# Kernel tuning notes

Hardware: AMD Instinct MI355X
Metric: run time of the kernel (lower is better)

Reference implementation:

```python
import jax, jax.numpy as jnp
import numpy as np

T, B, S = 64, 128, 128
H = 200   # hidden_size
E = 200   # embedding_size
A = 100   # attention projection width
V = 10003 # vocab_size


def setup_inputs() -> dict:
    key = jax.random.key(0)
    ks = jax.random.split(key, 20)
    def n(k, shape, scale):
        return (jax.random.normal(k, shape, jnp.float32) * scale).astype(jnp.float32)
    return {
        "tokens": jax.random.randint(ks[0], (T, B), 0, V),
        "hidden": n(ks[1], (1, B, H), 0.1),
        "encoder_outputs": n(ks[2], (S, B, H), 1.0),
        "emb": n(ks[3], (V, E), 0.05),
        "W1": n(ks[4], (A, H), 0.07), "b1": n(ks[5], (A,), 0.07),
        "W2": n(ks[6], (A, H), 0.07), "b2": n(ks[7], (A,), 0.07),
        "W3": n(ks[8], (A, E), 0.07), "b3": n(ks[9], (A,), 0.07),
        "attn_W": n(ks[10], (1, A), 0.1), "attn_b": n(ks[11], (1,), 0.1),
        "gru_Wih": n(ks[12], (3 * H, E + H), 0.05), "gru_Whh": n(ks[13], (3 * H, H), 0.05),
        "gru_bih": n(ks[14], (3 * H,), 0.05), "gru_bhh": n(ks[15], (3 * H,), 0.05),
        "out_W": n(ks[16], (V, H), 0.05), "out_b": n(ks[17], (V,), 0.05),
    }


def reference(tokens, hidden, encoder_outputs, emb, W1, b1, W2, b2, W3, b3,
              attn_W, attn_b, gru_Wih, gru_Whh, gru_bih, gru_bhh, out_W, out_b):
    # eval mode: dropout is identity
    enc = jnp.transpose(encoder_outputs, (1, 0, 2))   # [B, S, H]
    embedded = emb[tokens]                            # [T, B, E]
    ah3 = embedded @ W3.T + b3                        # [T, B, A] (precomputed, as in torch)
    ah2 = enc @ W2.T + b2                             # [B, S, A]
    h0 = hidden[0]                                    # [B, H]

    def step(h, xs):
        emb_t, ah3_t = xs                             # [B,E], [B,A]
        ah1 = h @ W1.T + b1                           # [B, A]
        e = jax.nn.relu(ah1[:, None, :] + ah2 + ah3_t[:, None, :])  # [B, S, A]
        logits = (e @ attn_W.T + attn_b)[..., 0]      # [B, S]
        a = jax.nn.softmax(logits, axis=1)            # [B, S]
        ctx = jnp.einsum('bs,bsh->bh', a, enc)        # [B, H]
        x = jnp.concatenate([emb_t, ctx], axis=1)     # [B, E+H]
        gi = x @ gru_Wih.T + gru_bih                  # [B, 3H]
        gh = h @ gru_Whh.T + gru_bhh                  # [B, 3H]
        ir, iz, in_ = jnp.split(gi, 3, axis=1)
        hr, hz, hn = jnp.split(gh, 3, axis=1)
        r = jax.nn.sigmoid(ir + hr)
        z = jax.nn.sigmoid(iz + hz)
        nn_ = jnp.tanh(in_ + r * hn)
        h_new = (1.0 - z) * nn_ + z * h               # [B, H]
        logp = jax.nn.log_softmax(h_new @ out_W.T + out_b, axis=1)  # [B, V]
        return h_new, (logp, a)

    h_last, (outputs, attns) = jax.lax.scan(step, h0, (embedded, ah3))
    # outputs [T,B,V]; hidden [1,B,H]; attentions [T,B,1,S] (torch's view(B,1,S) per step)
    return outputs, h_last[None], attns[:, :, None, :]
```

## Files before the change

### kernel.cpp

```cpp
#include <hip/hip_runtime.h>
#include <hip/hip_bf16.h>
#include <cmath>

constexpr int T_ = 64, B_ = 128, S_ = 128, H_ = 200, E_ = 200, A_ = 100, V_ = 10003;
constexpr int KP = 224;
constexpr int VP = 10240;
constexpr int MROWS = T_ * B_;
constexpr int NCB = VP / 256;
constexpr int G3 = 3 * H_;
constexpr int EH = E_ + H_;
constexpr int ELD = 136;
constexpr int AH2P = 104;
constexpr int NP = 768;

typedef __attribute__((ext_vector_type(8))) short bf16x8;
typedef __attribute__((ext_vector_type(4))) float f32x4;
typedef __attribute__((ext_vector_type(2))) _Float16 h2;
typedef __attribute__((ext_vector_type(8))) _Float16 h8;

#if __has_builtin(__builtin_amdgcn_fdot2)
__device__ __forceinline__ float fdot2f(h2 a, h2 b, float c) {
  return __builtin_amdgcn_fdot2(a, b, c, false);
}
#else
__device__ __forceinline__ float fdot2f(h2 a, h2 b, float c) {
  return c + (float)a[0] * (float)b[0] + (float)a[1] * (float)b[1];
}
#endif

__device__ __forceinline__ float dot200p5(const h8* __restrict__ w, int stride,
                                          const h8* __restrict__ x) {
  const h8* p = w;
  h8 w0 = p[0]; p += stride;
  h8 w1 = p[0]; p += stride;
  h8 w2 = p[0]; p += stride;
  h8 w3 = p[0]; p += stride;
  h8 w4 = p[0]; p += stride;
  float a0 = 0.f, a1 = 0.f, a2 = 0.f, a3 = 0.f;
#define DOT_CONSUME(WREG, K)                    \
  {                                             \
    h8 xv = x[K];                               \
    h2 wp[4], xp[4];                            \
    __builtin_memcpy(wp, &WREG, 16);            \
    __builtin_memcpy(xp, &xv, 16);              \
    a0 = fdot2f(wp[0], xp[0], a0);              \
    a1 = fdot2f(wp[1], xp[1], a1);              \
    a2 = fdot2f(wp[2], xp[2], a2);              \
    a3 = fdot2f(wp[3], xp[3], a3);              \
  }
#define DOT_RELOAD(WREG) { WREG = p[0]; p += stride; }
  DOT_CONSUME(w0, 0)  DOT_RELOAD(w0)
  DOT_CONSUME(w1, 1)  DOT_RELOAD(w1)
  DOT_CONSUME(w2, 2)  DOT_RELOAD(w2)
  DOT_CONSUME(w3, 3)  DOT_RELOAD(w3)
  DOT_CONSUME(w4, 4)  DOT_RELOAD(w4)
  DOT_CONSUME(w0, 5)  DOT_RELOAD(w0)
  DOT_CONSUME(w1, 6)  DOT_RELOAD(w1)
  DOT_CONSUME(w2, 7)  DOT_RELOAD(w2)
  DOT_CONSUME(w3, 8)  DOT_RELOAD(w3)
  DOT_CONSUME(w4, 9)  DOT_RELOAD(w4)
  DOT_CONSUME(w0, 10) DOT_RELOAD(w0)
  DOT_CONSUME(w1, 11) DOT_RELOAD(w1)
  DOT_CONSUME(w2, 12) DOT_RELOAD(w2)
  DOT_CONSUME(w3, 13) DOT_RELOAD(w3)
  DOT_CONSUME(w4, 14) DOT_RELOAD(w4)
  DOT_CONSUME(w0, 15) DOT_RELOAD(w0)
  DOT_CONSUME(w1, 16) DOT_RELOAD(w1)
  DOT_CONSUME(w2, 17) DOT_RELOAD(w2)
  DOT_CONSUME(w3, 18) DOT_RELOAD(w3)
  DOT_CONSUME(w4, 19) DOT_RELOAD(w4)
  DOT_CONSUME(w0, 20)
  DOT_CONSUME(w1, 21)
  DOT_CONSUME(w2, 22)
  DOT_CONSUME(w3, 23)
  DOT_CONSUME(w4, 24)
#undef DOT_CONSUME
#undef DOT_RELOAD
  return (a0 + a1) + (a2 + a3);
}


__global__ __launch_bounds__(256) void k_pack(const float* __restrict__ outW,
                                              const float* __restrict__ W1,
                                              const float* __restrict__ Wih,
                                              const float* __restrict__ Whh,
                                              const float* __restrict__ W3,
                                              __hip_bfloat16* __restrict__ wpk,
                                              __hip_bfloat16* __restrict__ hall,
                                              _Float16* __restrict__ W1h,
                                              _Float16* __restrict__ Wihh,
                                              _Float16* __restrict__ Whhh,
                                              __hip_bfloat16* __restrict__ wep) {
  const int stride = gridDim.x * blockDim.x;
  const int tid0 = blockIdx.x * blockDim.x + threadIdx.x;
  const int total = (KP / 8) * VP * 8;
  for (int idx = tid0; idx < total; idx += stride) {
    int kk = idx & 7;
    int v = (idx >> 3) % VP;
    int kb = idx / (8 * VP);
    int k = kb * 8 + kk;
    float val = (k < H_ && v < V_) ? outW[(size_t)v * H_ + k] : 0.f;
    wpk[idx] = __float2bfloat16(val);
  }
  const __hip_bfloat16 z = __float2bfloat16(0.f);
  for (int idx = tid0; idx < MROWS * (KP - H_); idx += stride) {
    int row = idx / (KP - H_), col = H_ + idx % (KP - H_);
    hall[(size_t)row * KP + col] = z;
  }
  for (int idx = tid0; idx < 25 * A_ * 8; idx += stride) {
    int kk = idx & 7, a = (idx >> 3) % A_, k8 = idx / (8 * A_);
    W1h[idx] = (_Float16)W1[(size_t)a * H_ + k8 * 8 + kk];
  }
  for (int idx = tid0; idx < 50 * G3 * 8; idx += stride) {
    int kk = idx & 7, n = (idx >> 3) % G3, k8 = idx / (8 * G3);
    Wihh[idx] = (_Float16)Wih[(size_t)n * EH + k8 * 8 + kk];
  }
  for (int idx = tid0; idx < 25 * G3 * 8; idx += stride) {
    int kk = idx & 7, n = (idx >> 3) % G3, k8 = idx / (8 * G3);
    Whhh[idx] = (_Float16)Whh[(size_t)n * H_ + k8 * 8 + kk];
  }
  for (int idx = tid0; idx < (KP / 8) * NP * 8; idx += stride) {
    int kk = idx & 7, c = (idx >> 3) % NP, k8 = idx / (8 * NP);
    int k = k8 * 8 + kk;
    float v = 0.f;
    if (k < E_) {
      if (c < G3) v = Wih[(size_t)c * EH + k];
      else if (c < G3 + A_) v = W3[(size_t)(c - G3) * E_ + k];
    }
    wep[idx] = __float2bfloat16(v);
  }
}

__global__ __launch_bounds__(256) void k_ah2(const float* __restrict__ encoder,
                                             const float* __restrict__ W2,
                                             const float* __restrict__ b2,
                                             _Float16* __restrict__ ah2h) {
  __shared__ float encL[16][200];
  const int s = blockIdx.x, b0 = blockIdx.y * 16, tid = threadIdx.x;
  for (int i = tid; i < 16 * 200; i += 256) {
    int bl = i / 200, k = i % 200;
    encL[bl][k] = encoder[((size_t)s * B_ + b0 + bl) * H_ + k];
  }
  __syncthreads();
  for (int o = tid; o < 16 * A_; o += 256) {
    int bl = o / A_, a = o % A_;
    const float* w = W2 + (size_t)a * H_;
    float acc = b2[a];
    for (int k = 0; k < H_; ++k) acc += encL[bl][k] * w[k];
    ah2h[((size_t)(b0 + bl) * S_ + s) * AH2P + a] = (_Float16)acc;
  }
  for (int o = tid; o < 16 * (AH2P - A_); o += 256) {
    int bl = o / (AH2P - A_), a = A_ + o % (AH2P - A_);
    ah2h[((size_t)(b0 + bl) * S_ + s) * AH2P + a] = (_Float16)0.f;
  }
}

__global__ __launch_bounds__(256) void k_gemb(const int* __restrict__ tokens,
                                              const float* __restrict__ emb,
                                              const short* __restrict__ wep,
                                              const float* __restrict__ bih,
                                              const float* __restrict__ b3,
                                              float* __restrict__ giX,
                                              float* __restrict__ ah3) {
  constexpr int ALD = 232;
  __shared__ __align__(16) __hip_bfloat16 aL[64 * ALD];
  __shared__ int tokL[64];
  const int tid = threadIdx.x;
  const int w = tid >> 6, l = tid & 63, lm = l & 15, lg = l >> 4;
  const int r0 = blockIdx.y * 64;
  const int v0 = blockIdx.x * 256 + w * 64;

  if (tid < 64) tokL[tid] = tokens[r0 + tid];
  __syncthreads();
  for (int i = tid; i < 64 * KP; i += 256) {
    int row = i / KP, k = i - row * KP;
    float v = (k < E_) ? emb[(size_t)tokL[row] * E_ + k] : 0.f;
    aL[row * ALD + k] = __float2bfloat16(v);
  }
  __syncthreads();

  f32x4 acc[4][4] = {};
#pragma unroll
  for (int kt = 0; kt < KP / 32; ++kt) {
    const int k0 = kt * 32;
    bf16x8 af[4], bfr[4];
#pragma unroll
    for (int wm = 0; wm < 4; ++wm)
      af[wm] = *(const bf16x8*)(aL + (wm * 16 + lm) * ALD + k0 + lg * 8);
#pragma unroll
    for (int n = 0; n < 4; ++n)
      bfr[n] = *(const bf16x8*)(wep + ((size_t)((k0 >> 3) + lg) * NP + v0 + n * 16 + lm) * 8);
#pragma unroll
    for (int wm = 0; wm < 4; ++wm)
#pragma unroll
      for (int n = 0; n < 4; ++n)
        acc[wm][n] = __builtin_amdgcn_mfma_f32_16x16x32_bf16(af[wm], bfr[n], acc[wm][n], 0, 0, 0);
  }

#pragma unroll
  for (int n = 0; n < 4; ++n) {
    const int vv = v0 + n * 16 + lm;
    const bool isGi = vv < G3;
    const bool isA3 = !isGi && vv < G3 + A_;
    const float bias = isGi ? bih[vv] : (isA3 ? b3[vv - G3] : 0.f);
#pragma unroll
    for (int wm = 0; wm < 4; ++wm) {
#pragma unroll
      for (int j = 0; j < 4; ++j) {
        const int row = r0 + wm * 16 + lg * 4 + j;
        const float val = acc[wm][n][j] + bias;
        if (isGi) giX[(size_t)row * G3 + vv] = val;
        else if (isA3) ah3[(size_t)row * A_ + (vv - G3)] = val;
      }
    }
  }
}

__global__ __launch_bounds__(512) void k_recur(const float* __restrict__ hidden0,
                                               const _Float16* __restrict__ ah2h,
                                               const float* __restrict__ ah3,
                                               const float* __restrict__ encoder,
                                               const _Float16* __restrict__ W1h,
                                               const float* __restrict__ b1,
                                               const float* __restrict__ attn_W,
                                               const float* __restrict__ attn_b,
                                               const _Float16* __restrict__ Wihh,
                                               const _Float16* __restrict__ Whhh,
                                               const float* __restrict__ bhh,
                                               const float* __restrict__ giX,
                                               __hip_bfloat16* __restrict__ hall,
                                               float* __restrict__ out_hidden,
                                               float* __restrict__ out_attn) {
  __shared__ __align__(16) _Float16 encLh[H_ * ELD];
  __shared__ __align__(16) h2 h16[100];
  __shared__ __align__(16) h2 xch[100];
  __shared__ __align__(16) h2 aLh[64];
  __shared__ float s1[AH2P];
  __shared__ float aW[AH2P];
  __shared__ float red[8];
  __shared__ float giL[G3];
  __shared__ float part[1200];

  const int b = blockIdx.x, tid = threadIdx.x;
  const int lane = tid & 63;

  for (int i = tid; i < S_ * H_; i += 512) {
    int s = i / H_, h = i - s * H_;
    encLh[h * ELD + s] = (_Float16)encoder[((size_t)s * B_ + b) * H_ + h];
  }
  float hreg = 0.f, bhr = 0.f, bhz = 0.f, bhn = 0.f;
  if (tid < H_) {
    hreg = hidden0[b * H_ + tid];
    bhr = bhh[tid]; bhz = bhh[200 + tid]; bhn = bhh[400 + tid];
  }
  if (tid < 100) {
    h2 v;
    v[0] = (_Float16)hidden0[b * H_ + 2 * tid];
    v[1] = (_Float16)hidden0[b * H_ + 2 * tid + 1];
    h16[tid] = v;
  }
  for (int i = tid; i < AH2P; i += 512) {
    aW[i] = (i < A_) ? attn_W[i] : 0.f;
    s1[i] = 0.f;
  }
  h8 ah2row[13];
  if (tid < S_) {
    const h8* src = (const h8*)(ah2h + ((size_t)b * S_ + tid) * AH2P);
#pragma unroll
    for (int r = 0; r < 13; ++r) ah2row[r] = src[r];
  }
  const float ab = attn_b[0];
  __syncthreads();

  const h8* W1h8 = (const h8*)W1h;
  const h8* Wihc8 = (const h8*)Wihh + (size_t)25 * G3;
  const h8* Whhh8 = (const h8*)Whhh;

  for (int t = 0; t < T_; ++t) {
    const h8* xs = (const h8*)h16;
    for (int u = tid; u < 700; u += 512) {
      if (u < 100) {
        const float ah3A = ah3[((size_t)t * B_ + b) * A_ + u];
        const float b1A = b1[u];
        s1[u] = dot200p5(W1h8 + u, A_, xs) + b1A + ah3A;
      } else {
        const int g = u - 100;
        part[g] = dot200p5(Whhh8 + g, G3, xs);
      }
    }
    __syncthreads();

    float evw = 0.f;
    const int w01 = tid >> 6;
    if (tid < S_) {
      float acc = ab;
#pragma unroll
      for (int r = 0; r < 13; ++r) {
        h8 w = ah2row[r];
#pragma unroll
        for (int j = 0; j < 8; ++j) {
          const int a = r * 8 + j;
          acc += fmaxf(s1[a] + (float)w[j], 0.f) * aW[a];
        }
      }
      float m = acc;
#pragma unroll
      for (int off = 32; off > 0; off >>= 1) m = fmaxf(m, __shfl_xor(m, off, 64));
      evw = expf(acc - m);
      float sm = evw;
#pragma unroll
      for (int off = 32; off > 0; off >>= 1) sm += __shfl_xor(sm, off, 64);
      if (lane == 0) { red[w01] = m; red[4 + w01] = sm; }
    }
    __syncthreads();
    if (tid < S_) {
      const float m0 = red[0], m1 = red[1];
      const float M = fmaxf(m0, m1);
      const float SS = red[4] * expf(m0 - M) + red[5] * expf(m1 - M);
      const float av = evw * expf((w01 ? m1 : m0) - M) / SS;
      out_attn[((size_t)t * B_ + b) * S_ + tid] = av;
      const float avn = __shfl_xor(av, 1, 64);
      if ((tid & 1) == 0) {
        h2 v; v[0] = (_Float16)av; v[1] = (_Float16)avn;
        aLh[tid >> 1] = v;
      }
    }
    __syncthreads();

    if (tid < H_) {
      const h8* er = (const h8*)(encLh + tid * ELD);
      float c0 = 0.f, c1 = 0.f, c2 = 0.f, c3 = 0.f;
#pragma unroll
      for (int k8 = 0; k8 < 16; ++k8) {
        h8 evv = er[k8];
        h2 ep[4];
        __builtin_memcpy(ep, &evv, 16);
        c0 = fdot2f(ep[0], aLh[4 * k8 + 0], c0);
        c1 = fdot2f(ep[1], aLh[4 * k8 + 1], c1);
        c2 = fdot2f(ep[2], aLh[4 * k8 + 2], c2);
        c3 = fdot2f(ep[3], aLh[4 * k8 + 3], c3);
      }
      const float c = (c0 + c1) + (c2 + c3);
      const float cn = __shfl_xor(c, 1, 64);
      if ((tid & 1) == 0) {
        h2 v; v[0] = (_Float16)c; v[1] = (_Float16)cn;
        xch[tid >> 1] = v;
      }
    } else {
      const int j = tid - 200;
      if (j < 300) {
        float2 g2 = ((const float2*)(giX + ((size_t)t * B_ + b) * G3))[j];
        giL[2 * j] = g2.x;
        giL[2 * j + 1] = g2.y;
      }
    }
    __syncthreads();

    {
      const h8* xc8 = (const h8*)xch;
      for (int u = tid; u < 600; u += 512) {
        part[600 + u] = dot200p5(Wihc8 + u, G3, xc8);
      }
    }
    __syncthreads();

    if (tid < H_) {
      const int n = tid;
      const float gir = giL[n] + part[600 + n];
      const float giz = giL[200 + n] + part[800 + n];
      const float gin = giL[400 + n] + part[1000 + n];
      const float ghr = part[n] + bhr;
      const float ghz = part[200 + n] + bhz;
      const float ghn = part[400 + n] + bhn;
      const float r = 1.f / (1.f + expf(-(gir + ghr)));
      const float z = 1.f / (1.f + expf(-(giz + ghz)));
      const float nn = tanhf(gin + r * ghn);
      const float hv = (1.f - z) * nn + z * hreg;
      hreg = hv;
      hall[((size_t)t * B_ + b) * KP + n] = __float2bfloat16(hv);
      const float hn2 = __shfl_xor(hv, 1, 64);
      if ((n & 1) == 0) {
        h2 v; v[0] = (_Float16)hv; v[1] = (_Float16)hn2;
        h16[n >> 1] = v;
      }
      if (t == T_ - 1) out_hidden[b * H_ + n] = hv;
    }
    __syncthreads();
  }
}

__global__ __launch_bounds__(256) void k_big0(const short* __restrict__ hb,
                                              const short* __restrict__ wpk,
                                              const float* __restrict__ outb,
                                              float* __restrict__ pmax,
                                              float* __restrict__ psum) {
  const int tid = threadIdx.x;
  const int w = tid >> 6, l = tid & 63;
  const int lm = l & 15, lg = l >> 4;
  const int r0 = blockIdx.y * 64;
  const int v0 = blockIdx.x * 256 + w * 64;

  f32x4 acc[4][4] = {};
#pragma unroll
  for (int kt = 0; kt < KP / 32; ++kt) {
    const int k0 = kt * 32;
    bf16x8 af[4], bfr[4];
#pragma unroll
    for (int wm = 0; wm < 4; ++wm)
      af[wm] = *(const bf16x8*)(hb + (size_t)(r0 + wm * 16 + lm) * KP + k0 + lg * 8);
#pragma unroll
    for (int n = 0; n < 4; ++n)
      bfr[n] = *(const bf16x8*)(wpk + ((size_t)((k0 >> 3) + lg) * VP + v0 + n * 16 + lm) * 8);
#pragma unroll
    for (int wm = 0; wm < 4; ++wm)
#pragma unroll
      for (int n = 0; n < 4; ++n)
        acc[wm][n] = __builtin_amdgcn_mfma_f32_16x16x32_bf16(af[wm], bfr[n], acc[wm][n], 0, 0, 0);
  }

  int vv[4]; float bias[4]; bool val[4];
#pragma unroll
  for (int n = 0; n < 4; ++n) {
    vv[n] = v0 + n * 16 + lm;
    val[n] = vv[n] < V_;
    bias[n] = val[n] ? outb[vv[n]] : 0.f;
  }

  __shared__ float smax[4][64], ssum[4][64];
#pragma unroll
  for (int wm = 0; wm < 4; ++wm) {
#pragma unroll
    for (int j = 0; j < 4; ++j) {
      float mv = -INFINITY;
#pragma unroll
      for (int n = 0; n < 4; ++n)
        if (val[n]) mv = fmaxf(mv, acc[wm][n][j] + bias[n]);
      for (int off = 8; off > 0; off >>= 1) mv = fmaxf(mv, __shfl_xor(mv, off, 64));
      float sv = 0.f;
#pragma unroll
      for (int n = 0; n < 4; ++n)
        if (val[n]) sv += expf(acc[wm][n][j] + bias[n] - mv);
      for (int off = 8; off > 0; off >>= 1) sv += __shfl_xor(sv, off, 64);
      if (lm == 0) {
        smax[w][wm * 16 + lg * 4 + j] = mv;
        ssum[w][wm * 16 + lg * 4 + j] = sv;
      }
    }
  }
  __syncthreads();
  if (tid < 64) {
    float mv = -INFINITY;
    for (int ww = 0; ww < 4; ++ww) mv = fmaxf(mv, smax[ww][tid]);
    float sv = 0.f;
    for (int ww = 0; ww < 4; ++ww) {
      float sw = ssum[ww][tid];
      if (sw > 0.f) sv += expf(smax[ww][tid] - mv) * sw;
    }
    pmax[(size_t)blockIdx.x * MROWS + r0 + tid] = mv;
    psum[(size_t)blockIdx.x * MROWS + r0 + tid] = sv;
  }
}

__global__ __launch_bounds__(256) void k_lse(const float* __restrict__ pmax,
                                             const float* __restrict__ psum,
                                             float* __restrict__ lse) {
  const int r = blockIdx.x * 256 + threadIdx.x;
  float mv = -INFINITY;
  for (int c = 0; c < NCB; ++c) mv = fmaxf(mv, pmax[(size_t)c * MROWS + r]);
  float sv = 0.f;
  for (int c = 0; c < NCB; ++c) {
    float sw = psum[(size_t)c * MROWS + r];
    if (sw > 0.f) sv += expf(pmax[(size_t)c * MROWS + r] - mv) * sw;
  }
  lse[r] = mv + logf(sv);
}

__global__ __launch_bounds__(256) void k_big1(const short* __restrict__ hb,
                                              const short* __restrict__ wpk,
                                              const float* __restrict__ outb,
                                              const float* __restrict__ lse,
                                              float* __restrict__ out_logp) {
  const int tid = threadIdx.x;
  const int w = tid >> 6, l = tid & 63;
  const int lm = l & 15, lg = l >> 4;
  const int r0 = blockIdx.y * 64;
  const int v0 = blockIdx.x * 256 + w * 64;

  __shared__ float lseL[64];
  if (tid < 64) lseL[tid] = lse[r0 + tid];

  f32x4 acc[4][4] = {};
#pragma unroll
  for (int kt = 0; kt < KP / 32; ++kt) {
    const int k0 = kt * 32;
    bf16x8 af[4], bfr[4];
#pragma unroll
    for (int wm = 0; wm < 4; ++wm)
      af[wm] = *(const bf16x8*)(hb + (size_t)(r0 + wm * 16 + lm) * KP + k0 + lg * 8);
#pragma unroll
    for (int n = 0; n < 4; ++n)
      bfr[n] = *(const bf16x8*)(wpk + ((size_t)((k0 >> 3) + lg) * VP + v0 + n * 16 + lm) * 8);
#pragma unroll
    for (int wm = 0; wm < 4; ++wm)
#pragma unroll
      for (int n = 0; n < 4; ++n)
        acc[wm][n] = __builtin_amdgcn_mfma_f32_16x16x32_bf16(af[wm], bfr[n], acc[wm][n], 0, 0, 0);
  }

  int vv[4]; float bias[4]; bool val[4];
#pragma unroll
  for (int n = 0; n < 4; ++n) {
    vv[n] = v0 + n * 16 + lm;
    val[n] = vv[n] < V_;
    bias[n] = val[n] ? outb[vv[n]] : 0.f;
  }
  __syncthreads();
#pragma unroll
  for (int wm = 0; wm < 4; ++wm) {
#pragma unroll
    for (int j = 0; j < 4; ++j) {
      const int row = r0 + wm * 16 + lg * 4 + j;
      const float ls = lseL[wm * 16 + lg * 4 + j];
#pragma unroll
      for (int n = 0; n < 4; ++n)
        if (val[n]) out_logp[(size_t)row * V_ + vv[n]] = acc[wm][n][j] + bias[n] - ls;
    }
  }
}


extern "C" void kernel_launch(void* const* d_in, const int* in_sizes, int n_in,
                              void* d_out, int out_size, void* d_ws, size_t ws_size,
                              hipStream_t stream) {
  (void)in_sizes; (void)n_in; (void)out_size; (void)ws_size;
  const int* tokens = (const int*)d_in[0];
  const float* hidden0 = (const float*)d_in[1];
  const float* encoder = (const float*)d_in[2];
  const float* emb = (const float*)d_in[3];
  const float* W1 = (const float*)d_in[4];
  const float* b1 = (const float*)d_in[5];
  const float* W2 = (const float*)d_in[6];
  const float* b2 = (const float*)d_in[7];
  const float* W3 = (const float*)d_in[8];
  const float* b3 = (const float*)d_in[9];
  const float* attn_W = (const float*)d_in[10];
  const float* attn_b = (const float*)d_in[11];
  const float* Wih = (const float*)d_in[12];
  const float* Whh = (const float*)d_in[13];
  const float* bih = (const float*)d_in[14];
  const float* bhh = (const float*)d_in[15];
  const float* outW = (const float*)d_in[16];
  const float* outb = (const float*)d_in[17];

  float* out_logp = (float*)d_out;
  float* out_hidden = out_logp + (size_t)T_ * B_ * V_;
  float* out_attn = out_hidden + (size_t)B_ * H_;

  float* ws = (float*)d_ws;
  float* ah3w = ws;
  float* pmaxw = ah3w + (size_t)T_ * B_ * A_;
  float* psumw = pmaxw + (size_t)NCB * MROWS;
  float* lsew = psumw + (size_t)NCB * MROWS;
  float* giXw = lsew + MROWS;
  __hip_bfloat16* hallw = (__hip_bfloat16*)(giXw + (size_t)MROWS * G3);
  __hip_bfloat16* wpkw = hallw + (size_t)MROWS * KP;
  _Float16* ah2hw = (_Float16*)(wpkw + (size_t)(KP / 8) * VP * 8);
  _Float16* W1hw = ah2hw + (size_t)B_ * S_ * AH2P;
  _Float16* Wihhw = W1hw + (size_t)25 * A_ * 8;
  _Float16* Whhhw = Wihhw + (size_t)50 * G3 * 8;
  __hip_bfloat16* wepw = (__hip_bfloat16*)(Whhhw + (size_t)25 * G3 * 8);

  k_pack<<<512, 256, 0, stream>>>(outW, W1, Wih, Whh, W3, wpkw, hallw,
                                  W1hw, Wihhw, Whhhw, wepw);
  k_ah2<<<dim3(S_, B_ / 16), 256, 0, stream>>>(encoder, W2, b2, ah2hw);
  k_gemb<<<dim3(NP / 256, MROWS / 64), 256, 0, stream>>>(tokens, emb, (const short*)wepw,
                                                         bih, b3, giXw, ah3w);

  k_recur<<<B_, 512, 0, stream>>>(hidden0, ah2hw, ah3w, encoder, W1hw, b1, attn_W,
                                  attn_b, Wihhw, Whhhw, bhh, giXw,
                                  hallw, out_hidden, out_attn);

  k_big0<<<dim3(NCB, MROWS / 64), 256, 0, stream>>>((const short*)hallw, (const short*)wpkw,
                                                    outb, pmaxw, psumw);
  k_lse<<<MROWS / 256, 256, 0, stream>>>(pmaxw, psumw, lsew);
  k_big1<<<dim3(NCB, MROWS / 64), 256, 0, stream>>>((const short*)hallw, (const short*)wpkw,
                                                    outb, lsew, out_logp);
}
```

Baseline: 1.033 ms.

## Overlap output-weight packing with recurrence and widen recurrent block to 640 threads

Moves the packing of the large output projection weights and the zeroing of hall padding out of k_pack and into 32 extra blocks of k_recur, so this work runs on otherwise idle CUs while the 128 serial recurrence blocks execute. The recurrence block grows from 512 to 640 threads, so each phase maps one unit per thread with no second strided pass. The leftover Whh gate dot products are computed by spare threads during the attention phase, and giX is loaded as float4. The risks are higher register pressure from the larger block and contention between the packing blocks and the recurrence for memory bandwidth.

```diff
diff --git a/kernel.cpp b/kernel.cpp
--- a/kernel.cpp
+++ b/kernel.cpp
@@ -12,6 +12,8 @@
 constexpr int ELD = 136;
 constexpr int AH2P = 104;
 constexpr int NP = 768;
+constexpr int NTH = 640;
+constexpr int NPK = 32;
 
 typedef __attribute__((ext_vector_type(8))) short bf16x8;
 typedef __attribute__((ext_vector_type(4))) float f32x4;
@@ -80,33 +82,16 @@
 }
 
 
-__global__ __launch_bounds__(256) void k_pack(const float* __restrict__ outW,
-                                              const float* __restrict__ W1,
+__global__ __launch_bounds__(256) void k_pack(const float* __restrict__ W1,
                                               const float* __restrict__ Wih,
                                               const float* __restrict__ Whh,
                                               const float* __restrict__ W3,
-                                              __hip_bfloat16* __restrict__ wpk,
-                                              __hip_bfloat16* __restrict__ hall,
                                               _Float16* __restrict__ W1h,
                                               _Float16* __restrict__ Wihh,
                                               _Float16* __restrict__ Whhh,
                                               __hip_bfloat16* __restrict__ wep) {
   const int stride = gridDim.x * blockDim.x;
   const int tid0 = blockIdx.x * blockDim.x + threadIdx.x;
-  const int total = (KP / 8) * VP * 8;
-  for (int idx = tid0; idx < total; idx += stride) {
-    int kk = idx & 7;
-    int v = (idx >> 3) % VP;
-    int kb = idx / (8 * VP);
-    int k = kb * 8 + kk;
-    float val = (k < H_ && v < V_) ? outW[(size_t)v * H_ + k] : 0.f;
-    wpk[idx] = __float2bfloat16(val);
-  }
-  const __hip_bfloat16 z = __float2bfloat16(0.f);
-  for (int idx = tid0; idx < MROWS * (KP - H_); idx += stride) {
-    int row = idx / (KP - H_), col = H_ + idx % (KP - H_);
-    hall[(size_t)row * KP + col] = z;
-  }
   for (int idx = tid0; idx < 25 * A_ * 8; idx += stride) {
     int kk = idx & 7, a = (idx >> 3) % A_, k8 = idx / (8 * A_);
     W1h[idx] = (_Float16)W1[(size_t)a * H_ + k8 * 8 + kk];
@@ -216,7 +201,7 @@
   }
 }
 
-__global__ __launch_bounds__(512) void k_recur(const float* __restrict__ hidden0,
+__global__ __launch_bounds__(NTH) void k_recur(const float* __restrict__ hidden0,
                                                const _Float16* __restrict__ ah2h,
                                                const float* __restrict__ ah3,
                                                const float* __restrict__ encoder,
@@ -228,6 +213,8 @@
                                                const _Float16* __restrict__ Whhh,
                                                const float* __restrict__ bhh,
                                                const float* __restrict__ giX,
+                                               const float* __restrict__ outW,
+                                               __hip_bfloat16* __restrict__ wpk,
                                                __hip_bfloat16* __restrict__ hall,
                                                float* __restrict__ out_hidden,
                                                float* __restrict__ out_attn) {
@@ -244,7 +231,27 @@
   const int b = blockIdx.x, tid = threadIdx.x;
   const int lane = tid & 63;
 
-  for (int i = tid; i < S_ * H_; i += 512) {
+  if (b >= B_) {
+    const int pt = (b - B_) * NTH + tid;
+    const int pstride = NPK * NTH;
+    const int total = (KP / 8) * VP * 8;
+    for (int idx = pt; idx < total; idx += pstride) {
+      int kk = idx & 7;
+      int v = (idx >> 3) % VP;
+      int kb = idx / (8 * VP);
+      int k = kb * 8 + kk;
+      float val = (k < H_ && v < V_) ? outW[(size_t)v * H_ + k] : 0.f;
+      wpk[idx] = __float2bfloat16(val);
+    }
+    const __hip_bfloat16 z = __float2bfloat16(0.f);
+    for (int idx = pt; idx < MROWS * (KP - H_); idx += pstride) {
+      int row = idx / (KP - H_), col = H_ + idx % (KP - H_);
+      hall[(size_t)row * KP + col] = z;
+    }
+    return;
+  }
+
+  for (int i = tid; i < S_ * H_; i += NTH) {
     int s = i / H_, h = i - s * H_;
     encLh[h * ELD + s] = (_Float16)encoder[((size_t)s * B_ + b) * H_ + h];
   }
@@ -259,7 +266,7 @@
     v[1] = (_Float16)hidden0[b * H_ + 2 * tid + 1];
     h16[tid] = v;
   }
-  for (int i = tid; i < AH2P; i += 512) {
+  for (int i = tid; i < AH2P; i += NTH) {
     aW[i] = (i < A_) ? attn_W[i] : 0.f;
     s1[i] = 0.f;
   }
@@ -278,15 +285,13 @@
 
   for (int t = 0; t < T_; ++t) {
     const h8* xs = (const h8*)h16;
-    for (int u = tid; u < 700; u += 512) {
-      if (u < 100) {
-        const float ah3A = ah3[((size_t)t * B_ + b) * A_ + u];
-        const float b1A = b1[u];
-        s1[u] = dot200p5(W1h8 + u, A_, xs) + b1A + ah3A;
-      } else {
-        const int g = u - 100;
-        part[g] = dot200p5(Whhh8 + g, G3, xs);
-      }
+    if (tid < 100) {
+      const float ah3A = ah3[((size_t)t * B_ + b) * A_ + tid];
+      const float b1A = b1[tid];
+      s1[tid] = dot200p5(W1h8 + tid, A_, xs) + b1A + ah3A;
+    } else {
+      const int g = tid - 100;
+      part[g] = dot200p5(Whhh8 + g, G3, xs);
     }
     __syncthreads();
 
@@ -346,21 +351,21 @@
         h2 v; v[0] = (_Float16)c; v[1] = (_Float16)cn;
         xch[tid >> 1] = v;
       }
-    } else {
+    } else if (tid < 350) {
       const int j = tid - 200;
-      if (j < 300) {
-        float2 g2 = ((const float2*)(giX + ((size_t)t * B_ + b) * G3))[j];
-        giL[2 * j] = g2.x;
-        giL[2 * j + 1] = g2.y;
-      }
+      float4 g4 = ((const float4*)(giX + ((size_t)t * B_ + b) * G3))[j];
+      giL[4 * j] = g4.x;
+      giL[4 * j + 1] = g4.y;
+      giL[4 * j + 2] = g4.z;
+      giL[4 * j + 3] = g4.w;
+    } else if (tid < 410) {
+      const int g = 540 + (tid - 350);
+      part[g] = dot200p5(Whhh8 + g, G3, xs);
     }
     __syncthreads();
 
-    {
-      const h8* xc8 = (const h8*)xch;
-      for (int u = tid; u < 600; u += 512) {
-        part[600 + u] = dot200p5(Wihc8 + u, G3, xc8);
-      }
+    if (tid < 600) {
+      part[600 + tid] = dot200p5(Wihc8 + tid, G3, (const h8*)xch);
     }
     __syncthreads();
 
@@ -570,15 +575,14 @@
   _Float16* Whhhw = Wihhw + (size_t)50 * G3 * 8;
   __hip_bfloat16* wepw = (__hip_bfloat16*)(Whhhw + (size_t)25 * G3 * 8);
 
-  k_pack<<<512, 256, 0, stream>>>(outW, W1, Wih, Whh, W3, wpkw, hallw,
-                                  W1hw, Wihhw, Whhhw, wepw);
+  k_pack<<<256, 256, 0, stream>>>(W1, Wih, Whh, W3, W1hw, Wihhw, Whhhw, wepw);
   k_ah2<<<dim3(S_, B_ / 16), 256, 0, stream>>>(encoder, W2, b2, ah2hw);
   k_gemb<<<dim3(NP / 256, MROWS / 64), 256, 0, stream>>>(tokens, emb, (const short*)wepw,
                                                          bih, b3, giXw, ah3w);
 
-  k_recur<<<B_, 512, 0, stream>>>(hidden0, ah2hw, ah3w, encoder, W1hw, b1, attn_W,
-                                  attn_b, Wihhw, Whhhw, bhh, giXw,
-                                  hallw, out_hidden, out_attn);
+  k_recur<<<B_ + NPK, NTH, 0, stream>>>(hidden0, ah2hw, ah3w, encoder, W1hw, b1, attn_W,
+                                        attn_b, Wihhw, Whhhw, bhh, giXw, outW, wpkw,
+                                        hallw, out_hidden, out_attn);
 
   k_big0<<<dim3(NCB, MROWS / 64), 256, 0, stream>>>((const short*)hallw, (const short*)wpkw,
                                                     outb, pmaxw, psumw);
```

Result: slower. 2.109 ms (+104.1%).

## Overlap output-weight packing with recurrence and use MFMA for encoder projection

Applied to the files above, without the earlier changes.

Packing of the large output-projection weights and zero-padding of the hidden buffer move out of the pre-pass kernel into 32 extra blocks of the recurrence kernel, so that work runs alongside the latency-bound recurrent loop. The scalar-FMA encoder projection kernel (ah2) is replaced with a bf16 MFMA GEMM over packed W2. This trades some precision (bf16 instead of fp32 for ah2) and adds packing blocks that compete with the recurrence blocks for resources.

```diff
diff --git a/kernel.cpp b/kernel.cpp
--- a/kernel.cpp
+++ b/kernel.cpp
@@ -12,6 +12,9 @@
 constexpr int ELD = 136;
 constexpr int AH2P = 104;
 constexpr int NP = 768;
+constexpr int NP2 = 128;
+constexpr int NTH = 512;
+constexpr int NPK = 32;
 
 typedef __attribute__((ext_vector_type(8))) short bf16x8;
 typedef __attribute__((ext_vector_type(4))) float f32x4;
@@ -80,33 +83,19 @@
 }
 
 
-__global__ __launch_bounds__(256) void k_pack(const float* __restrict__ outW,
-                                              const float* __restrict__ W1,
+__global__ __launch_bounds__(256) void k_pack(const float* __restrict__ W1,
                                               const float* __restrict__ Wih,
                                               const float* __restrict__ Whh,
                                               const float* __restrict__ W3,
-                                              __hip_bfloat16* __restrict__ wpk,
-                                              __hip_bfloat16* __restrict__ hall,
+                                              const float* __restrict__ W2,
                                               _Float16* __restrict__ W1h,
                                               _Float16* __restrict__ Wihh,
                                               _Float16* __restrict__ Whhh,
-                                              __hip_bfloat16* __restrict__ wep) {
+                                              __hip_bfloat16* __restrict__ wep,
+                                              __hip_bfloat16* __restrict__ w2p,
+                                              _Float16* __restrict__ ah2h) {
   const int stride = gridDim.x * blockDim.x;
   const int tid0 = blockIdx.x * blockDim.x + threadIdx.x;
-  const int total = (KP / 8) * VP * 8;
-  for (int idx = tid0; idx < total; idx += stride) {
-    int kk = idx & 7;
-    int v = (idx >> 3) % VP;
-    int kb = idx / (8 * VP);
-    int k = kb * 8 + kk;
-    float val = (k < H_ && v < V_) ? outW[(size_t)v * H_ + k] : 0.f;
-    wpk[idx] = __float2bfloat16(val);
-  }
-  const __hip_bfloat16 z = __float2bfloat16(0.f);
-  for (int idx = tid0; idx < MROWS * (KP - H_); idx += stride) {
-    int row = idx / (KP - H_), col = H_ + idx % (KP - H_);
-    hall[(size_t)row * KP + col] = z;
-  }
   for (int idx = tid0; idx < 25 * A_ * 8; idx += stride) {
     int kk = idx & 7, a = (idx >> 3) % A_, k8 = idx / (8 * A_);
     W1h[idx] = (_Float16)W1[(size_t)a * H_ + k8 * 8 + kk];
@@ -129,29 +118,70 @@
     }
     wep[idx] = __float2bfloat16(v);
   }
-}
-
-__global__ __launch_bounds__(256) void k_ah2(const float* __restrict__ encoder,
-                                             const float* __restrict__ W2,
-                                             const float* __restrict__ b2,
-                                             _Float16* __restrict__ ah2h) {
-  __shared__ float encL[16][200];
-  const int s = blockIdx.x, b0 = blockIdx.y * 16, tid = threadIdx.x;
-  for (int i = tid; i < 16 * 200; i += 256) {
-    int bl = i / 200, k = i % 200;
-    encL[bl][k] = encoder[((size_t)s * B_ + b0 + bl) * H_ + k];
+  for (int idx = tid0; idx < (KP / 8) * NP2 * 8; idx += stride) {
+    int kk = idx & 7, c = (idx >> 3) % NP2, k8 = idx / (8 * NP2);
+    int k = k8 * 8 + kk;
+    float v = (k < H_ && c < A_) ? W2[(size_t)c * H_ + k] : 0.f;
+    w2p[idx] = __float2bfloat16(v);
+  }
+  for (int idx = tid0; idx < B_ * S_ * (AH2P - A_); idx += stride) {
+    int row = idx / (AH2P - A_), col = A_ + idx % (AH2P - A_);
+    ah2h[(size_t)row * AH2P + col] = (_Float16)0.f;
+  }
+}
+
+__global__ __launch_bounds__(256) void k_genc(const float* __restrict__ encoder,
+                                              const short* __restrict__ w2p,
+                                              const float* __restrict__ b2,
+                                              _Float16* __restrict__ ah2h) {
+  constexpr int ALD = 232;
+  __shared__ __align__(16) __hip_bfloat16 aL[128 * ALD];
+  const int tid = threadIdx.x;
+  const int w = tid >> 6, l = tid & 63, lm = l & 15, lg = l >> 4;
+  const int r0 = blockIdx.y * 128;
+  const int rloc = (w >> 1) * 64;
+  const int v0 = (w & 1) * 64;
+
+  for (int i = tid; i < 128 * KP; i += 256) {
+    int row = i / KP, k = i - row * KP;
+    float v = (k < H_) ? encoder[(size_t)(r0 + row) * H_ + k] : 0.f;
+    aL[row * ALD + k] = __float2bfloat16(v);
   }
   __syncthreads();
-  for (int o = tid; o < 16 * A_; o += 256) {
-    int bl = o / A_, a = o % A_;
-    const float* w = W2 + (size_t)a * H_;
-    float acc = b2[a];
-    for (int k = 0; k < H_; ++k) acc += encL[bl][k] * w[k];
-    ah2h[((size_t)(b0 + bl) * S_ + s) * AH2P + a] = (_Float16)acc;
-  }
-  for (int o = tid; o < 16 * (AH2P - A_); o += 256) {
-    int bl = o / (AH2P - A_), a = A_ + o % (AH2P - A_);
-    ah2h[((size_t)(b0 + bl) * S_ + s) * AH2P + a] = (_Float16)0.f;
+
+  f32x4 acc[4][4] = {};
+#pragma unroll
+  for (int kt = 0; kt < KP / 32; ++kt) {
+    const int k0 = kt * 32;
+    bf16x8 af[4], bfr[4];
+#pragma unroll
+    for (int wm = 0; wm < 4; ++wm)
+      af[wm] = *(const bf16x8*)(aL + (rloc + wm * 16 + lm) * ALD + k0 + lg * 8);
+#pragma unroll
+    for (int n = 0; n < 4; ++n)
+      bfr[n] = *(const bf16x8*)(w2p + ((size_t)((k0 >> 3) + lg) * NP2 + v0 + n * 16 + lm) * 8);
+#pragma unroll
+    for (int wm = 0; wm < 4; ++wm)
+#pragma unroll
+      for (int n = 0; n < 4; ++n)
+        acc[wm][n] = __builtin_amdgcn_mfma_f32_16x16x32_bf16(af[wm], bfr[n], acc[wm][n], 0, 0, 0);
+  }
+
+#pragma unroll
+  for (int n = 0; n < 4; ++n) {
+    const int vv = v0 + n * 16 + lm;
+    if (vv >= A_) continue;
+    const float bias = b2[vv];
+#pragma unroll
+    for (int wm = 0; wm < 4; ++wm) {
+#pragma unroll
+      for (int j = 0; j < 4; ++j) {
+        const int grow = r0 + rloc + wm * 16 + lg * 4 + j;
+        const int bb = grow & (B_ - 1);
+        const int ss = grow >> 7;
+        ah2h[((size_t)bb * S_ + ss) * AH2P + vv] = (_Float16)(acc[wm][n][j] + bias);
+      }
+    }
   }
 }
 
@@ -216,7 +246,7 @@
   }
 }
 
-__global__ __launch_bounds__(512) void k_recur(const float* __restrict__ hidden0,
+__global__ __launch_bounds__(NTH) void k_recur(const float* __restrict__ hidden0,
                                                const _Float16* __restrict__ ah2h,
                                                const float* __restrict__ ah3,
                                                const float* __restrict__ encoder,
@@ -228,6 +258,8 @@
                                                const _Float16* __restrict__ Whhh,
                                                const float* __restrict__ bhh,
                                                const float* __restrict__ giX,
+                                               const float* __restrict__ outW,
+                                               __hip_bfloat16* __restrict__ wpk,
                                                __hip_bfloat16* __restrict__ hall,
                                                float* __restrict__ out_hidden,
                                                float* __restrict__ out_attn) {
@@ -244,7 +276,27 @@
   const int b = blockIdx.x, tid = threadIdx.x;
   const int lane = tid & 63;
 
-  for (int i = tid; i < S_ * H_; i += 512) {
+  if (b >= B_) {
+    const int pt = (b - B_) * NTH + tid;
+    const int pstride = NPK * NTH;
+    const int total = (KP / 8) * VP * 8;
+    for (int idx = pt; idx < total; idx += pstride) {
+      int kk = idx & 7;
+      int v = (idx >> 3) % VP;
+      int kb = idx / (8 * VP);
+      int k = kb * 8 + kk;
+      float val = (k < H_ && v < V_) ? outW[(size_t)v * H_ + k] : 0.f;
+      wpk[idx] = __float2bfloat16(val);
+    }
+    const __hip_bfloat16 z = __float2bfloat16(0.f);
+    for (int idx = pt; idx < MROWS * (KP - H_); idx += pstride) {
+      int row = idx / (KP - H_), col = H_ + idx % (KP - H_);
+      hall[(size_t)row * KP + col] = z;
+    }
+    return;
+  }
+
+  for (int i = tid; i < S_ * H_; i += NTH) {
     int s = i / H_, h = i - s * H_;
     encLh[h * ELD + s] = (_Float16)encoder[((size_t)s * B_ + b) * H_ + h];
   }
@@ -259,7 +311,7 @@
     v[1] = (_Float16)hidden0[b * H_ + 2 * tid + 1];
     h16[tid] = v;
   }
-  for (int i = tid; i < AH2P; i += 512) {
+  for (int i = tid; i < AH2P; i += NTH) {
     aW[i] = (i < A_) ? attn_W[i] : 0.f;
     s1[i] = 0.f;
   }
@@ -278,7 +330,7 @@
 
   for (int t = 0; t < T_; ++t) {
     const h8* xs = (const h8*)h16;
-    for (int u = tid; u < 700; u += 512) {
+    for (int u = tid; u < 700; u += NTH) {
       if (u < 100) {
         const float ah3A = ah3[((size_t)t * B_ + b) * A_ + u];
         const float b1A = b1[u];
@@ -358,7 +410,7 @@
 
     {
       const h8* xc8 = (const h8*)xch;
-      for (int u = tid; u < 600; u += 512) {
+      for (int u = tid; u < 600; u += NTH) {
         part[600 + u] = dot200p5(Wihc8 + u, G3, xc8);
       }
     }
@@ -569,16 +621,18 @@
   _Float16* Wihhw = W1hw + (size_t)25 * A_ * 8;
   _Float16* Whhhw = Wihhw + (size_t)50 * G3 * 8;
   __hip_bfloat16* wepw = (__hip_bfloat16*)(Whhhw + (size_t)25 * G3 * 8);
-
-  k_pack<<<512, 256, 0, stream>>>(outW, W1, Wih, Whh, W3, wpkw, hallw,
-                                  W1hw, Wihhw, Whhhw, wepw);
-  k_ah2<<<dim3(S_, B_ / 16), 256, 0, stream>>>(encoder, W2, b2, ah2hw);
+  __hip_bfloat16* w2pw = wepw + (size_t)(KP / 8) * NP * 8;
+
+  k_pack<<<256, 256, 0, stream>>>(W1, Wih, Whh, W3, W2,
+                                  W1hw, Wihhw, Whhhw, wepw, w2pw, ah2hw);
+  k_genc<<<dim3(1, S_ * B_ / 128), 256, 0, stream>>>(encoder, (const short*)w2pw,
+                                                     b2, ah2hw);
   k_gemb<<<dim3(NP / 256, MROWS / 64), 256, 0, stream>>>(tokens, emb, (const short*)wepw,
                                                          bih, b3, giXw, ah3w);
 
-  k_recur<<<B_, 512, 0, stream>>>(hidden0, ah2hw, ah3w, encoder, W1hw, b1, attn_W,
-                                  attn_b, Wihhw, Whhhw, bhh, giXw,
-                                  hallw, out_hidden, out_attn);
+  k_recur<<<B_ + NPK, NTH, 0, stream>>>(hidden0, ah2hw, ah3w, encoder, W1hw, b1, attn_W,
+                                        attn_b, Wihhw, Whhhw, bhh, giXw, outW, wpkw,
+                                        hallw, out_hidden, out_attn);
 
   k_big0<<<dim3(NCB, MROWS / 64), 256, 0, stream>>>((const short*)hallw, (const short*)wpkw,
                                                     outb, pmaxw, psumw);
```

After: 996.6 us. -3.5%, faster.
